# Optimization experiments

Hardware: AMD Instinct MI355X
Metric: run time of the kernel (lower is better)

## Reference

```python
import jax, jax.numpy as jnp
import numpy as np

VOCAB = 50000
EMBED = 256
BATCH = 16384
NUM_SAMPLED = 4096


def _log_uniform_prob(ids):
    # P(c) = (log(c+2) - log(c+1)) / log(V+1), the log-uniform sampler distribution
    ids = ids.astype(jnp.float32)
    return (jnp.log(ids + 2.0) - jnp.log(ids + 1.0)) / jnp.log(VOCAB + 1.0)


def _expected_count(ids, num_sampled):
    # unique log-uniform sampler expected count: 1 - (1 - p)^num_tries, num_tries ~= num_sampled
    p = _log_uniform_prob(ids)
    return -jnp.expm1(num_sampled * jnp.log1p(-p))


def _sigmoid_xent(logits, labels):
    # stable sigmoid cross-entropy: max(x,0) - x*z + log(1 + exp(-|x|))
    return jnp.maximum(logits, 0.0) - logits * labels + jnp.log1p(jnp.exp(-jnp.abs(logits)))


def setup_inputs() -> dict:
    key = jax.random.key(0)
    k1, k2, k3, k4 = jax.random.split(key, 4)
    embedding = jax.random.normal(k1, (BATCH, EMBED), dtype=jnp.float32)
    target_words = jax.random.randint(k2, (BATCH, 1), 0, VOCAB, dtype=jnp.int64 if jax.config.jax_enable_x64 else jnp.int32)
    sampled_ids = jax.random.randint(k3, (NUM_SAMPLED,), 0, VOCAB, dtype=jnp.int64 if jax.config.jax_enable_x64 else jnp.int32)
    # truncated-normal init with stddev 1/sqrt(embed_size), matching TruncatedNormal
    nce_weight = (jax.random.truncated_normal(k4, -2.0, 2.0, (VOCAB, EMBED), dtype=jnp.float32)
                  * (1.0 / EMBED ** 0.5))
    nce_bias = jnp.zeros((VOCAB,), dtype=jnp.float32)
    return {"embedding": embedding, "target_words": target_words,
            "sampled_ids": sampled_ids, "nce_weight": nce_weight, "nce_bias": nce_bias}


def reference(embedding, target_words, sampled_ids, nce_weight, nce_bias):
    num_sampled = sampled_ids.shape[0]
    labels = target_words[:, 0]                       # [B]

    # gather true-class rows and compute true logits (subtract_log_q=True in tf.nn.nce_loss)
    w_true = nce_weight[labels]                       # [B, D]
    true_logits = (jnp.sum(embedding * w_true, axis=-1) + nce_bias[labels]
                   - jnp.log(_expected_count(labels, num_sampled)))          # [B]

    # gather sampled rows and compute sampled logits
    w_samp = nce_weight[sampled_ids]                  # [S, D]
    sampled_logits = (jnp.einsum('bd,sd->bs', embedding, w_samp) + nce_bias[sampled_ids]
                      - jnp.log(_expected_count(sampled_ids, num_sampled)))  # [B, S]

    # sigmoid cross-entropy: true label 1, sampled labels 0; sum per example, mean over batch
    per_example = _sigmoid_xent(true_logits, 1.0) + jnp.sum(_sigmoid_xent(sampled_logits, 0.0), axis=-1)
    return jnp.mean(per_example)
```

## Files before the change

kernel.cpp:

```cpp
#include <hip/hip_runtime.h>
#include <cstdint>
#include <cstddef>

#define VOCAB 50000
#define EMBED 256
#define BATCH 16384
#define NSAMP 4096

typedef float f32x4 __attribute__((ext_vector_type(4)));
typedef int   i32x8 __attribute__((ext_vector_type(8)));


__device__ __forceinline__ f32x4 vsplat(float a) {
    f32x4 r = {a, a, a, a};
    return r;
}

__device__ __forceinline__ float log_expected_count(int id) {
    float u = 1.0f / ((float)id + 1.0f);
    float a = __logf(1.0f + u);
    float p = a * 0.09242324f;
    float ser = p * (1.0f + p * (0.5f + p * (0.33333333f + p * (0.25f + p * 0.2f))));
    float q = -(float)NSAMP * ser;
    return __logf(1.0f - __expf(q));
}

__device__ __forceinline__ float softplus_f(float x) {
    float v = __expf(-fabsf(x));
    float p = fmaf(v, 0.03215845f, -0.13606275f);
    p = fmaf(v, p, 0.28947478f);
    p = fmaf(v, p, -0.49190896f);
    p = fmaf(v, p, 0.99949556f);
    return fmaxf(x, 0.0f) + v * p;
}

__device__ __forceinline__ void softplus4_acc(f32x4 x, f32x4& vsum) {
    f32x4 ax = __builtin_elementwise_abs(x);
    f32x4 v;
    v.x = __expf(-ax.x);
    v.y = __expf(-ax.y);
    v.z = __expf(-ax.z);
    v.w = __expf(-ax.w);
    f32x4 p = __builtin_elementwise_fma(v, vsplat(0.03215845f), vsplat(-0.13606275f));
    p = __builtin_elementwise_fma(v, p, vsplat(0.28947478f));
    p = __builtin_elementwise_fma(v, p, vsplat(-0.49190896f));
    p = __builtin_elementwise_fma(v, p, vsplat(0.99949556f));
    vsum += __builtin_elementwise_max(x, vsplat(0.0f));
    vsum = __builtin_elementwise_fma(v, p, vsum);
}

__device__ __forceinline__ int pk4_fp8(float a, float b, float c, float d) {
    int v = __builtin_amdgcn_cvt_pk_fp8_f32(a, b, 0, false);
    v = __builtin_amdgcn_cvt_pk_fp8_f32(c, d, v, true);
    return v;
}



__global__ __launch_bounds__(256) void k_prep(
        const float* __restrict__ E, const int* __restrict__ tgt,
        const int* __restrict__ sids, const float* __restrict__ W,
        const float* __restrict__ bias,
        unsigned char* __restrict__ EF, unsigned char* __restrict__ BF,
        float* __restrict__ badj, double* __restrict__ pTrue)
{
    const int blk = blockIdx.x, tid = threadIdx.x;
    const int wave = tid >> 6, lane = tid & 63;

    if (blk < 1024) {
        float tsum = 0.0f;
        #pragma unroll
        for (int i = 0; i < 4; ++i) {
            int b = (blk * 4 + wave) + 4096 * i;
            int label = tgt[b];
            float4 e  = ((const float4*)(E + (size_t)b * EMBED))[lane];
            float4 wv = ((const float4*)(W + (size_t)label * EMBED))[lane];
            int pk = pk4_fp8(e.x, e.y, e.z, e.w);
            *(int*)(EF + ((b >> 4) * 4096 + (lane >> 3) * 512
                          + (b & 15) * 32 + (lane & 7) * 4)) = pk;
            float d = e.x * wv.x + e.y * wv.y + e.z * wv.z + e.w * wv.w;
            #pragma unroll
            for (int off = 32; off > 0; off >>= 1) d += __shfl_down(d, off, 64);
            if (lane == 0) {
                float tl = d + bias[label] - log_expected_count(label);
                tsum += softplus_f(-tl);
            }
        }
        __shared__ float ts[4];
        if (lane == 0) ts[wave] = tsum;
        __syncthreads();
        if (tid == 0) pTrue[blk] = (double)((ts[0] + ts[1]) + (ts[2] + ts[3]));
    } else {
        #pragma unroll
        for (int i = 0; i < 4; ++i) {
            int task = (blk - 1024) * 256 + tid + 16384 * i;
            int s = task >> 4, p = task & 15;
            int sid = sids[s];
            const float4* wr = (const float4*)(W + (size_t)sid * EMBED + p * 16);
            float4 w0 = wr[0], w1 = wr[1], w2 = wr[2], w3 = wr[3];
            int4 o;
            o.x = pk4_fp8(w0.x * 16.0f, w0.y * 16.0f, w0.z * 16.0f, w0.w * 16.0f);
            o.y = pk4_fp8(w1.x * 16.0f, w1.y * 16.0f, w1.z * 16.0f, w1.w * 16.0f);
            o.z = pk4_fp8(w2.x * 16.0f, w2.y * 16.0f, w2.z * 16.0f, w2.w * 16.0f);
            o.w = pk4_fp8(w3.x * 16.0f, w3.y * 16.0f, w3.z * 16.0f, w3.w * 16.0f);
            *(int4*)(BF + ((s >> 4) * 4096 + (p >> 1) * 512
                           + (s & 15) * 32 + (p & 1) * 16)) = o;
            if (p == 0) badj[s] = bias[sid] - log_expected_count(sid);
        }
    }
}

__global__ __launch_bounds__(256, 2) void k_gemm(
        const unsigned char* __restrict__ EF,
        const unsigned char* __restrict__ BF,
        const float* __restrict__ badj,
        double* __restrict__ pGemm)
{
    const int tid  = threadIdx.x;
    const int wave = tid >> 6;
    const int lane = tid & 63;
    const int rg   = blockIdx.x >> 4;
    const int cg   = blockIdx.x & 15;
    const int ag0  = rg * 16 + wave * 4;
    const int r16  = lane & 15;

    i32x8 af[2][4];
    #pragma unroll
    for (int s = 0; s < 2; ++s)
        #pragma unroll
        for (int mi = 0; mi < 4; ++mi)
            af[s][mi] = *(const i32x8*)(EF + (size_t)(ag0 + mi) * 4096
                                        + s * 2048 + lane * 32);

#define LOAD_B(bf, ba, j) do {                                              \
        const int bg0_ = cg * 16 + (j) * 4;                                 \
        _Pragma("unroll")                                                   \
        for (int s_ = 0; s_ < 2; ++s_)                                      \
            _Pragma("unroll")                                               \
            for (int ni_ = 0; ni_ < 4; ++ni_)                               \
                bf[s_][ni_] = *(const i32x8*)(BF + (size_t)(bg0_ + ni_) * 4096 \
                                              + s_ * 2048 + lane * 32);     \
        _Pragma("unroll")                                                   \
        for (int ni_ = 0; ni_ < 4; ++ni_)                                   \
            ba[ni_] = badj[cg * 256 + (j) * 64 + ni_ * 16 + r16];           \
    } while (0)

#define COMPUTE_J(bf, ba) do {                                              \
        _Pragma("unroll")                                                   \
        for (int mi_ = 0; mi_ < 4; ++mi_) {                                 \
            f32x4 acc[4] = {};                                              \
            _Pragma("unroll")                                               \
            for (int s_ = 0; s_ < 2; ++s_)                                  \
                _Pragma("unroll")                                           \
                for (int ni_ = 0; ni_ < 4; ++ni_)                           \
                    acc[ni_] = __builtin_amdgcn_mfma_scale_f32_16x16x128_f8f6f4( \
                        af[s_][mi_], bf[s_][ni_], acc[ni_],                 \
                        0, 0,                       \
                        0, 0x7F7F7F7F,                   \
                        0, 0x7B7B7B7B);                 \
            _Pragma("unroll")                                               \
            for (int ni_ = 0; ni_ < 4; ++ni_)                               \
                softplus4_acc(acc[ni_] + ba[ni_], vsum);                    \
        }                                                                   \
    } while (0)

    i32x8 bfA[2][4], bfB[2][4];
    float baA[4], baB[4];

    LOAD_B(bfA, baA, 0);
    LOAD_B(bfB, baB, 1);

    #pragma unroll
    for (int s = 0; s < 2; ++s)
        #pragma unroll
        for (int mi = 0; mi < 4; ++mi)
            asm volatile("" : "+v"(af[s][mi]));

    f32x4 vsum = {};

    COMPUTE_J(bfA, baA);
    LOAD_B(bfA, baA, 2);
    COMPUTE_J(bfB, baB);
    LOAD_B(bfB, baB, 3);
    COMPUTE_J(bfA, baA);
    COMPUTE_J(bfB, baB);

#undef LOAD_B
#undef COMPUTE_J

    float lsum = (vsum.x + vsum.y) + (vsum.z + vsum.w);
    #pragma unroll
    for (int off = 32; off > 0; off >>= 1) lsum += __shfl_down(lsum, off, 64);
    __shared__ float wsum[4];
    if (lane == 0) wsum[wave] = lsum;
    __syncthreads();
    if (tid == 0)
        pGemm[blockIdx.x] = (double)((wsum[0] + wsum[1]) + (wsum[2] + wsum[3]));
}

__global__ __launch_bounds__(256) void k_final(
        const double* __restrict__ pTrue, const double* __restrict__ pGemm,
        float* __restrict__ out)
{
    const int tid = threadIdx.x, wave = tid >> 6, lane = tid & 63;
    double s = 0.0;
    for (int i = tid; i < 1024; i += 256) s += pTrue[i];
    for (int i = tid; i < 1024; i += 256) s += pGemm[i];
    #pragma unroll
    for (int off = 32; off > 0; off >>= 1) s += __shfl_down(s, off, 64);
    __shared__ double wsum[4];
    if (lane == 0) wsum[wave] = s;
    __syncthreads();
    if (tid == 0)
        out[0] = (float)(((wsum[0] + wsum[1]) + (wsum[2] + wsum[3]))
                         * (1.0 / (double)BATCH));
}


extern "C" void kernel_launch(void* const* d_in, const int* in_sizes, int n_in,
                              void* d_out, int out_size, void* d_ws, size_t ws_size,
                              hipStream_t stream) {
    const float* emb  = (const float*)d_in[0];
    const int*   tgt  = (const int*)d_in[1];
    const int*   sids = (const int*)d_in[2];
    const float* W    = (const float*)d_in[3];
    const float* bias = (const float*)d_in[4];
    float* out = (float*)d_out;

    char* ws = (char*)d_ws;
    double*        pTrue = (double*)ws;
    double*        pGemm = (double*)(ws + 8192);
    float*         badj  = (float*)(ws + 40960);
    unsigned char* BF    = (unsigned char*)(ws + 57344);
    unsigned char* EF    = (unsigned char*)(ws + 57344 + 1048576);

    hipLaunchKernelGGL(k_prep, dim3(1088), dim3(256), 0, stream,
                       emb, tgt, sids, W, bias, EF, BF, badj, pTrue);
    hipLaunchKernelGGL(k_gemm, dim3(1024), dim3(256), 0, stream,
                       EF, BF, badj, pGemm);
    hipLaunchKernelGGL(k_final, dim3(1), dim3(256), 0, stream,
                       pTrue, pGemm, out);
}
```

Baseline: 132.7 us.

## Stage sampled-weight tiles in LDS via async global_load_lds with 8-wave blocks

The GEMM kernel now copies each block's 64 KB fp8 sampled-weight tile into LDS with asynchronous global_load_lds and reads B fragments from LDS. Previously every wave fetched B from global memory itself. Blocks grow to 512 threads (8 waves, 2 row groups each), and the BF layout in the prep kernel is reordered so LDS reads are conflict-friendly 16-byte halves. This reduces redundant global/L2 traffic for B across waves. The cost is LDS capacity, which limits occupancy, and per-chunk barriers with vmcnt waits.

Result: no change. 131.1 us (-1.2%).

```diff
diff --git a/kernel.cpp b/kernel.cpp
--- a/kernel.cpp
+++ b/kernel.cpp
@@ -8,6 +8,7 @@
 #define NSAMP 4096
 
 typedef float f32x4 __attribute__((ext_vector_type(4)));
+typedef int   i32x4 __attribute__((ext_vector_type(4)));
 typedef int   i32x8 __attribute__((ext_vector_type(8)));
 
 
@@ -103,14 +104,14 @@
             o.y = pk4_fp8(w1.x * 16.0f, w1.y * 16.0f, w1.z * 16.0f, w1.w * 16.0f);
             o.z = pk4_fp8(w2.x * 16.0f, w2.y * 16.0f, w2.z * 16.0f, w2.w * 16.0f);
             o.w = pk4_fp8(w3.x * 16.0f, w3.y * 16.0f, w3.z * 16.0f, w3.w * 16.0f);
-            *(int4*)(BF + ((s >> 4) * 4096 + (p >> 1) * 512
-                           + (s & 15) * 32 + (p & 1) * 16)) = o;
+            *(int4*)(BF + ((s >> 4) * 4096 + (p >> 1) * 512 + (p & 1) * 256
+                           + (s & 15) * 16)) = o;
             if (p == 0) badj[s] = bias[sid] - log_expected_count(sid);
         }
     }
 }
 
-__global__ __launch_bounds__(256, 2) void k_gemm(
+__global__ __launch_bounds__(512, 4) void k_gemm(
         const unsigned char* __restrict__ EF,
         const unsigned char* __restrict__ BF,
         const float* __restrict__ badj,
@@ -121,33 +122,66 @@
     const int lane = tid & 63;
     const int rg   = blockIdx.x >> 4;
     const int cg   = blockIdx.x & 15;
-    const int ag0  = rg * 16 + wave * 4;
+    const int ag0  = rg * 16 + wave * 2;
     const int r16  = lane & 15;
 
-    i32x8 af[2][4];
+    __shared__ unsigned char Blds[65536];
+    __shared__ float wsum[8];
+
+    i32x8 af[2][2];
     #pragma unroll
     for (int s = 0; s < 2; ++s)
         #pragma unroll
-        for (int mi = 0; mi < 4; ++mi)
+        for (int mi = 0; mi < 2; ++mi)
             af[s][mi] = *(const i32x8*)(EF + (size_t)(ag0 + mi) * 4096
                                         + s * 2048 + lane * 32);
 
-#define LOAD_B(bf, ba, j) do {                                              \
-        const int bg0_ = cg * 16 + (j) * 4;                                 \
+    {
+        const unsigned char* Bsrc = BF + (size_t)cg * 65536;
+        #pragma unroll
+        for (int it = 0; it < 8; ++it) {
+            int woff = it * 8192 + wave * 1024;
+            int goff = woff + lane * 16;
+            __builtin_amdgcn_global_load_lds(
+                (const __attribute__((address_space(1))) void*)(Bsrc + goff),
+                (__attribute__((address_space(3))) void*)(Blds + woff),
+                16, 0, 0);
+        }
+    }
+
+    #pragma unroll
+    for (int s = 0; s < 2; ++s)
+        #pragma unroll
+        for (int mi = 0; mi < 2; ++mi)
+            asm volatile("" : "+v"(af[s][mi]));
+
+    f32x4 vsum = {};
+    const int lbase = (lane >> 4) * 512 + r16 * 16;
+
+#define COMPUTE_J(J, VM) do {                                               \
+        asm volatile("s_waitcnt vmcnt(" #VM ")" ::: "memory");              \
+        __builtin_amdgcn_s_barrier();                                       \
+        __builtin_amdgcn_sched_barrier(0);                                  \
+        i32x8 bf[2][4];                                                     \
         _Pragma("unroll")                                                   \
         for (int s_ = 0; s_ < 2; ++s_)                                      \
             _Pragma("unroll")                                               \
-            for (int ni_ = 0; ni_ < 4; ++ni_)                               \
-                bf[s_][ni_] = *(const i32x8*)(BF + (size_t)(bg0_ + ni_) * 4096 \
-                                              + s_ * 2048 + lane * 32);     \
+            for (int ni_ = 0; ni_ < 4; ++ni_) {                             \
+                const unsigned char* bp = Blds + ((J) * 4 + ni_) * 4096     \
+                                          + s_ * 2048 + lbase;              \
+                i32x4 lo = *(const i32x4*)bp;                               \
+                i32x4 hi = *(const i32x4*)(bp + 256);                       \
+                bf[s_][ni_][0] = lo[0]; bf[s_][ni_][1] = lo[1];             \
+                bf[s_][ni_][2] = lo[2]; bf[s_][ni_][3] = lo[3];             \
+                bf[s_][ni_][4] = hi[0]; bf[s_][ni_][5] = hi[1];             \
+                bf[s_][ni_][6] = hi[2]; bf[s_][ni_][7] = hi[3];             \
+            }                                                               \
+        float ba[4];                                                        \
         _Pragma("unroll")                                                   \
         for (int ni_ = 0; ni_ < 4; ++ni_)                                   \
-            ba[ni_] = badj[cg * 256 + (j) * 64 + ni_ * 16 + r16];           \
-    } while (0)
-
-#define COMPUTE_J(bf, ba) do {                                              \
+            ba[ni_] = badj[cg * 256 + (J) * 64 + ni_ * 16 + r16];           \
         _Pragma("unroll")                                                   \
-        for (int mi_ = 0; mi_ < 4; ++mi_) {                                 \
+        for (int mi_ = 0; mi_ < 2; ++mi_) {                                 \
             f32x4 acc[4] = {};                                              \
             _Pragma("unroll")                                               \
             for (int s_ = 0; s_ < 2; ++s_)                                  \
@@ -160,42 +194,25 @@
                         0, 0x7B7B7B7B);                 \
             _Pragma("unroll")                                               \
             for (int ni_ = 0; ni_ < 4; ++ni_)                               \
-                softplus4_acc(acc[ni_] + ba[ni_], vsum);                    \
+                softplus4_acc(acc[ni_] + vsplat(ba[ni_]), vsum);            \
         }                                                                   \
     } while (0)
 
-    i32x8 bfA[2][4], bfB[2][4];
-    float baA[4], baB[4];
-
-    LOAD_B(bfA, baA, 0);
-    LOAD_B(bfB, baB, 1);
-
-    #pragma unroll
-    for (int s = 0; s < 2; ++s)
-        #pragma unroll
-        for (int mi = 0; mi < 4; ++mi)
-            asm volatile("" : "+v"(af[s][mi]));
-
-    f32x4 vsum = {};
-
-    COMPUTE_J(bfA, baA);
-    LOAD_B(bfA, baA, 2);
-    COMPUTE_J(bfB, baB);
-    LOAD_B(bfB, baB, 3);
-    COMPUTE_J(bfA, baA);
-    COMPUTE_J(bfB, baB);
-
-#undef LOAD_B
+    COMPUTE_J(0, 6);
+    COMPUTE_J(1, 4);
+    COMPUTE_J(2, 2);
+    COMPUTE_J(3, 0);
+
 #undef COMPUTE_J
 
     float lsum = (vsum.x + vsum.y) + (vsum.z + vsum.w);
     #pragma unroll
     for (int off = 32; off > 0; off >>= 1) lsum += __shfl_down(lsum, off, 64);
-    __shared__ float wsum[4];
     if (lane == 0) wsum[wave] = lsum;
     __syncthreads();
     if (tid == 0)
-        pGemm[blockIdx.x] = (double)((wsum[0] + wsum[1]) + (wsum[2] + wsum[3]));
+        pGemm[blockIdx.x] = (double)((((wsum[0] + wsum[1]) + (wsum[2] + wsum[3]))
+                                    + ((wsum[4] + wsum[5]) + (wsum[6] + wsum[7]))));
 }
 
 __global__ __launch_bounds__(256) void k_final(
@@ -236,7 +253,7 @@
 
     hipLaunchKernelGGL(k_prep, dim3(1088), dim3(256), 0, stream,
                        emb, tgt, sids, W, bias, EF, BF, badj, pTrue);
-    hipLaunchKernelGGL(k_gemm, dim3(1024), dim3(256), 0, stream,
+    hipLaunchKernelGGL(k_gemm, dim3(1024), dim3(512), 0, stream,
                        EF, BF, badj, pGemm);
     hipLaunchKernelGGL(k_final, dim3(1), dim3(256), 0, stream,
                        pTrue, pGemm, out);
```
